# Kernel optimization log

Hardware: AMD Instinct MI355X
Metric: run time of the kernel (lower is better)

## Reference

```python
import jax, jax.numpy as jnp
import numpy as np

SPARSITY = 0.15
GAIN = 3.0

def setup_inputs() -> dict:
    key = jax.random.key(0)
    x = jax.random.normal(key, (16384, 4096), dtype=jnp.float32)
    return {"x": x}

def reference(x):
    N, D = x.shape
    k = max(int(D * SPARSITY), 2)
    topk_values, topk_indices = jax.lax.top_k(x, k)  # [N, k]
    diff = topk_values[:, 0] - topk_values[:, 1]      # [N]
    dynamic_gain = (jax.nn.sigmoid(diff) * GAIN + 1.0)[:, None]  # [N, 1]
    rows = jnp.arange(N)[:, None]
    mask = jnp.zeros_like(x).at[rows, topk_indices].set(1.0)
    return x * mask * dynamic_gain
```

## Files before the change

kernel.cpp:

```cpp
#include <hip/hip_runtime.h>
#include <math.h>


#define D      4096
#define K      614
#define BLOCK  256
#define NWAVES 4

__device__ __forceinline__ unsigned int f2ord(float f) {
    unsigned int b = __float_as_uint(f);
    return (b & 0x80000000u) ? ~b : (b | 0x80000000u);
}
__device__ __forceinline__ float ord2f(unsigned int u) {
    unsigned int b = (u & 0x80000000u) ? (u ^ 0x80000000u) : ~u;
    return __uint_as_float(b);
}

__global__ __launch_bounds__(BLOCK, 1)
void diffgated_topk(const float* __restrict__ x, float* __restrict__ out) {
    const int row  = blockIdx.x;
    const int tid  = threadIdx.x;
    const int wave = tid >> 6;
    const int lane = tid & 63;
    const float* xrow = x + (size_t)row * D;
    float*       orow = out + (size_t)row * D;

    __shared__ unsigned int u_lds[D];
    __shared__ int hist[NWAVES][256];
    __shared__ int scan_s[256];
    __shared__ unsigned int sh_prefix;
    __shared__ int sh_krem, sh_numeq, sh_eqbase;
    __shared__ float sh_w1[NWAVES], sh_w2[NWAVES], sh_gain;
    __shared__ int sh_wsum[NWAVES];

    #pragma unroll
    for (int w = 0; w < NWAVES; ++w) hist[w][tid] = 0;
    if (tid == 0) { sh_prefix = 0u; sh_krem = K; sh_eqbase = 0; }
    __syncthreads();

    float m1 = -INFINITY, m2 = -INFINITY;
    for (int i = tid; i < D / 4; i += BLOCK) {
        float4 v = ((const float4*)xrow)[i];
        float vs[4] = { v.x, v.y, v.z, v.w };
        uint4 uu;
        unsigned int* up = (unsigned int*)&uu;
        #pragma unroll
        for (int j = 0; j < 4; ++j) {
            float f = vs[j];
            if (f > m1) { m2 = m1; m1 = f; } else if (f > m2) { m2 = f; }
            unsigned int u = f2ord(f);
            up[j] = u;
            atomicAdd(&hist[wave][u >> 24], 1);
        }
        ((uint4*)u_lds)[i] = uu;
    }

    #pragma unroll
    for (int off = 32; off > 0; off >>= 1) {
        float o1 = __shfl_down(m1, off);
        float o2 = __shfl_down(m2, off);
        float hi = fmaxf(m1, o1);
        float lo = fminf(m1, o1);
        m2 = fmaxf(lo, fmaxf(m2, o2));
        m1 = hi;
    }
    if (lane == 0) { sh_w1[wave] = m1; sh_w2[wave] = m2; }
    __syncthreads();
    if (tid == 0) {
        float a1 = sh_w1[0], a2 = sh_w2[0];
        #pragma unroll
        for (int w = 1; w < NWAVES; ++w) {
            float b1 = sh_w1[w], b2 = sh_w2[w];
            float hi = fmaxf(a1, b1), lo = fminf(a1, b1);
            a2 = fmaxf(lo, fmaxf(a2, b2));
            a1 = hi;
        }
        float diff = a1 - a2;
        float sig  = 1.0f / (1.0f + expf(-diff));
        sh_gain = sig * 3.0f + 1.0f;
    }

    for (int pass = 0; pass < 4; ++pass) {
        const int shift = 24 - 8 * pass;
        int csum = hist[0][tid] + hist[1][tid] + hist[2][tid] + hist[3][tid];
        scan_s[tid] = csum;
        __syncthreads();
        for (int off = 1; off < 256; off <<= 1) {
            int v = (tid + off < 256) ? scan_s[tid + off] : 0;
            __syncthreads();
            scan_s[tid] += v;
            __syncthreads();
        }
        int S = scan_s[tid];
        int krem = sh_krem;
        __syncthreads();
        if (S >= krem && S - csum < krem) {
            sh_prefix |= ((unsigned int)tid) << shift;
            sh_krem = krem - (S - csum);
            sh_numeq = csum;
        }
        __syncthreads();
        if (pass < 3) {
            #pragma unroll
            for (int w = 0; w < NWAVES; ++w) hist[w][tid] = 0;
            __syncthreads();
            const unsigned int pfx = sh_prefix;
            const int shift2 = shift - 8;
            for (int i = tid; i < D / 4; i += BLOCK) {
                uint4 uu = ((const uint4*)u_lds)[i];
                const unsigned int* up = (const unsigned int*)&uu;
                #pragma unroll
                for (int j = 0; j < 4; ++j) {
                    unsigned int u = up[j];
                    if (((u ^ pfx) >> shift) == 0)
                        atomicAdd(&hist[wave][(u >> shift2) & 0xFF], 1);
                }
            }
            __syncthreads();
        }
    }

    const float gain        = sh_gain;
    const unsigned int ut   = sh_prefix;
    const int needed        = sh_krem;
    const int numeq         = sh_numeq;

    if (numeq == needed) {
        for (int i = tid; i < D / 4; i += BLOCK) {
            uint4 uu = ((const uint4*)u_lds)[i];
            const unsigned int* up = (const unsigned int*)&uu;
            float4 o;
            float* op = (float*)&o;
            #pragma unroll
            for (int j = 0; j < 4; ++j) {
                unsigned int u = up[j];
                op[j] = (u >= ut) ? ord2f(u) * gain : 0.0f;
            }
            ((float4*)orow)[i] = o;
        }
    } else {
        for (int c0 = 0; c0 < D; c0 += BLOCK) {
            unsigned int u = u_lds[c0 + tid];
            bool eq = (u == ut);
            unsigned long long bal = __ballot(eq);
            if (lane == 0) sh_wsum[wave] = __popcll(bal);
            __syncthreads();
            int before = sh_eqbase;
            for (int w = 0; w < wave; ++w) before += sh_wsum[w];
            int myrank = before + __popcll(bal & ((1ull << lane) - 1ull));
            float f = 0.0f;
            if (u > ut || (eq && myrank < needed)) f = ord2f(u) * gain;
            orow[c0 + tid] = f;
            __syncthreads();
            if (tid == 0) {
                int s = 0;
                #pragma unroll
                for (int w = 0; w < NWAVES; ++w) s += sh_wsum[w];
                sh_eqbase += s;
            }
            __syncthreads();
        }
    }
}

extern "C" void kernel_launch(void* const* d_in, const int* in_sizes, int n_in,
                              void* d_out, int out_size, void* d_ws, size_t ws_size,
                              hipStream_t stream) {
    const float* x = (const float*)d_in[0];
    float* out = (float*)d_out;
    const int rows = in_sizes[0] / D;
    diffgated_topk<<<dim3(rows), dim3(BLOCK), 0, stream>>>(x, out);
}
```

Measured before the change: 489.9 us.

## Process one row per wavefront with register-resident values and ballot bisection

Each 64-lane wavefront now owns a whole row and keeps its 4096 values in registers (64 per lane), so the shared-memory copy, LDS histograms, block-wide scans and most barriers are gone. The k-th threshold comes from a 32-step binary search over the ordered-uint key space, where each step counts elements with ballot and popcount. Tie ranking uses ballot masks across the wavefront. The cost is heavy register pressure and 32 search iterations of 64 ballots each per row, traded against the removed synchronisation and LDS atomics.

```diff
diff --git a/kernel.cpp b/kernel.cpp
--- a/kernel.cpp
+++ b/kernel.cpp
@@ -2,10 +2,11 @@
 #include <math.h>
 
 
-#define D      4096
-#define K      614
-#define BLOCK  256
-#define NWAVES 4
+#define D     4096
+#define K     614
+#define BLOCK 256
+#define VPT   64
+#define NB    16
 
 __device__ __forceinline__ unsigned int f2ord(float f) {
     unsigned int b = __float_as_uint(f);
@@ -16,149 +17,100 @@
     return __uint_as_float(b);
 }
 
-__global__ __launch_bounds__(BLOCK, 1)
-void diffgated_topk(const float* __restrict__ x, float* __restrict__ out) {
-    const int row  = blockIdx.x;
-    const int tid  = threadIdx.x;
-    const int wave = tid >> 6;
-    const int lane = tid & 63;
+__global__ __launch_bounds__(BLOCK, 5)
+void diffgated_topk(const float* __restrict__ x, float* __restrict__ out, int rows) {
+    const int lane = threadIdx.x & 63;
+    const int wav  = threadIdx.x >> 6;
+    const int row  = blockIdx.x * 4 + wav;
+    if (row >= rows) return;
     const float* xrow = x + (size_t)row * D;
     float*       orow = out + (size_t)row * D;
 
-    __shared__ unsigned int u_lds[D];
-    __shared__ int hist[NWAVES][256];
-    __shared__ int scan_s[256];
-    __shared__ unsigned int sh_prefix;
-    __shared__ int sh_krem, sh_numeq, sh_eqbase;
-    __shared__ float sh_w1[NWAVES], sh_w2[NWAVES], sh_gain;
-    __shared__ int sh_wsum[NWAVES];
-
+    unsigned int u[VPT];
+    float m1 = -INFINITY, m2 = -INFINITY;
     #pragma unroll
-    for (int w = 0; w < NWAVES; ++w) hist[w][tid] = 0;
-    if (tid == 0) { sh_prefix = 0u; sh_krem = K; sh_eqbase = 0; }
-    __syncthreads();
-
-    float m1 = -INFINITY, m2 = -INFINITY;
-    for (int i = tid; i < D / 4; i += BLOCK) {
-        float4 v = ((const float4*)xrow)[i];
+    for (int b = 0; b < NB; ++b) {
+        float4 v = ((const float4*)xrow)[b * 64 + lane];
         float vs[4] = { v.x, v.y, v.z, v.w };
-        uint4 uu;
-        unsigned int* up = (unsigned int*)&uu;
         #pragma unroll
         for (int j = 0; j < 4; ++j) {
             float f = vs[j];
             if (f > m1) { m2 = m1; m1 = f; } else if (f > m2) { m2 = f; }
-            unsigned int u = f2ord(f);
-            up[j] = u;
-            atomicAdd(&hist[wave][u >> 24], 1);
+            u[b * 4 + j] = f2ord(f);
         }
-        ((uint4*)u_lds)[i] = uu;
     }
 
     #pragma unroll
-    for (int off = 32; off > 0; off >>= 1) {
-        float o1 = __shfl_down(m1, off);
-        float o2 = __shfl_down(m2, off);
-        float hi = fmaxf(m1, o1);
-        float lo = fminf(m1, o1);
-        m2 = fmaxf(lo, fmaxf(m2, o2));
+    for (int off = 32; off; off >>= 1) {
+        float o1 = __shfl_xor(m1, off);
+        float o2 = __shfl_xor(m2, off);
+        float hi = fmaxf(m1, o1), lo2 = fminf(m1, o1);
+        m2 = fmaxf(lo2, fmaxf(m2, o2));
         m1 = hi;
     }
-    if (lane == 0) { sh_w1[wave] = m1; sh_w2[wave] = m2; }
-    __syncthreads();
-    if (tid == 0) {
-        float a1 = sh_w1[0], a2 = sh_w2[0];
+    const float gain = 1.0f / (1.0f + expf(-(m1 - m2))) * 3.0f + 1.0f;
+
+    unsigned long long lo = 0ull, hi = 0x100000000ull;
+    for (int it = 0; it < 32; ++it) {
+        unsigned int mid = (unsigned int)((lo + hi) >> 1);
+        int cnt = 0;
         #pragma unroll
-        for (int w = 1; w < NWAVES; ++w) {
-            float b1 = sh_w1[w], b2 = sh_w2[w];
-            float hi = fmaxf(a1, b1), lo = fminf(a1, b1);
-            a2 = fmaxf(lo, fmaxf(a2, b2));
-            a1 = hi;
-        }
-        float diff = a1 - a2;
-        float sig  = 1.0f / (1.0f + expf(-diff));
-        sh_gain = sig * 3.0f + 1.0f;
+        for (int j = 0; j < VPT; ++j)
+            cnt += (int)__popcll(__ballot(u[j] >= mid));
+        if (cnt >= K) lo = mid; else hi = mid;
     }
+    const unsigned int ut = (unsigned int)lo;
 
-    for (int pass = 0; pass < 4; ++pass) {
-        const int shift = 24 - 8 * pass;
-        int csum = hist[0][tid] + hist[1][tid] + hist[2][tid] + hist[3][tid];
-        scan_s[tid] = csum;
-        __syncthreads();
-        for (int off = 1; off < 256; off <<= 1) {
-            int v = (tid + off < 256) ? scan_s[tid + off] : 0;
-            __syncthreads();
-            scan_s[tid] += v;
-            __syncthreads();
-        }
-        int S = scan_s[tid];
-        int krem = sh_krem;
-        __syncthreads();
-        if (S >= krem && S - csum < krem) {
-            sh_prefix |= ((unsigned int)tid) << shift;
-            sh_krem = krem - (S - csum);
-            sh_numeq = csum;
-        }
-        __syncthreads();
-        if (pass < 3) {
-            #pragma unroll
-            for (int w = 0; w < NWAVES; ++w) hist[w][tid] = 0;
-            __syncthreads();
-            const unsigned int pfx = sh_prefix;
-            const int shift2 = shift - 8;
-            for (int i = tid; i < D / 4; i += BLOCK) {
-                uint4 uu = ((const uint4*)u_lds)[i];
-                const unsigned int* up = (const unsigned int*)&uu;
-                #pragma unroll
-                for (int j = 0; j < 4; ++j) {
-                    unsigned int u = up[j];
-                    if (((u ^ pfx) >> shift) == 0)
-                        atomicAdd(&hist[wave][(u >> shift2) & 0xFF], 1);
-                }
-            }
-            __syncthreads();
-        }
+    int cnt_gt = 0, cnt_eq = 0;
+    #pragma unroll
+    for (int j = 0; j < VPT; ++j) {
+        cnt_gt += (int)__popcll(__ballot(u[j] >  ut));
+        cnt_eq += (int)__popcll(__ballot(u[j] == ut));
     }
+    const int needed = K - cnt_gt;
 
-    const float gain        = sh_gain;
-    const unsigned int ut   = sh_prefix;
-    const int needed        = sh_krem;
-    const int numeq         = sh_numeq;
-
-    if (numeq == needed) {
-        for (int i = tid; i < D / 4; i += BLOCK) {
-            uint4 uu = ((const uint4*)u_lds)[i];
-            const unsigned int* up = (const unsigned int*)&uu;
-            float4 o;
-            float* op = (float*)&o;
+    if (cnt_eq == needed) {
+        #pragma unroll
+        for (int b = 0; b < NB; ++b) {
+            float4 o; float* op = (float*)&o;
             #pragma unroll
             for (int j = 0; j < 4; ++j) {
-                unsigned int u = up[j];
-                op[j] = (u >= ut) ? ord2f(u) * gain : 0.0f;
+                unsigned int uu = u[b * 4 + j];
+                op[j] = (uu >= ut) ? ord2f(uu) * gain : 0.0f;
             }
-            ((float4*)orow)[i] = o;
+            ((float4*)orow)[b * 64 + lane] = o;
         }
     } else {
-        for (int c0 = 0; c0 < D; c0 += BLOCK) {
-            unsigned int u = u_lds[c0 + tid];
-            bool eq = (u == ut);
-            unsigned long long bal = __ballot(eq);
-            if (lane == 0) sh_wsum[wave] = __popcll(bal);
-            __syncthreads();
-            int before = sh_eqbase;
-            for (int w = 0; w < wave; ++w) before += sh_wsum[w];
-            int myrank = before + __popcll(bal & ((1ull << lane) - 1ull));
-            float f = 0.0f;
-            if (u > ut || (eq && myrank < needed)) f = ord2f(u) * gain;
-            orow[c0 + tid] = f;
-            __syncthreads();
-            if (tid == 0) {
-                int s = 0;
-                #pragma unroll
-                for (int w = 0; w < NWAVES; ++w) s += sh_wsum[w];
-                sh_eqbase += s;
+        const unsigned long long ltmask =
+            (lane == 0) ? 0ull : ((~0ull) >> (64 - lane));
+        int eq_before = 0;
+        #pragma unroll
+        for (int b = 0; b < NB; ++b) {
+            unsigned long long bal[4];
+            #pragma unroll
+            for (int j = 0; j < 4; ++j) bal[j] = __ballot(u[b * 4 + j] == ut);
+            float4 o; float* op = (float*)&o;
+            #pragma unroll
+            for (int j = 0; j < 4; ++j) {
+                unsigned int uu = u[b * 4 + j];
+                float f = 0.0f;
+                if (uu > ut) {
+                    f = ord2f(uu) * gain;
+                } else if (uu == ut) {
+                    int r = eq_before;
+                    #pragma unroll
+                    for (int j2 = 0; j2 < 4; ++j2) {
+                        r += (int)__popcll(bal[j2] & ltmask);
+                        if (j2 < j) r += (int)((bal[j2] >> lane) & 1ull);
+                    }
+                    if (r < needed) f = ord2f(uu) * gain;
+                }
+                op[j] = f;
             }
-            __syncthreads();
+            ((float4*)orow)[b * 64 + lane] = o;
+            #pragma unroll
+            for (int j2 = 0; j2 < 4; ++j2)
+                eq_before += (int)__popcll(bal[j2]);
         }
     }
 }
@@ -169,5 +121,5 @@
     const float* x = (const float*)d_in[0];
     float* out = (float*)d_out;
     const int rows = in_sizes[0] / D;
-    diffgated_topk<<<dim3(rows), dim3(BLOCK), 0, stream>>>(x, out);
+    diffgated_topk<<<dim3((rows + 3) / 4), dim3(BLOCK), 0, stream>>>(x, out, rows);
 }
```

New measurement: 530.5 us. 1.08x slower.
